# Kernel tuning notes

Measured on AMD Instinct MI355X. Metric: run time of the kernel, lower is better.

## Reference

```python
import jax, jax.numpy as jnp
import numpy as np

NUM_CLASSES = 1000  # label vocabulary size (matches fill_max for label)
B = 16384
D_IN = 1024   # image_embedding
D_OUT = 256   # projection_dim


def setup_inputs() -> dict:
    key = jax.random.key(0)
    k = jax.random.split(key, 6)
    x = jax.random.normal(k[0], (B, D_IN), dtype=jnp.float32)
    label = jax.random.randint(k[1], (B,), 0, NUM_CLASSES, dtype=jnp.int64)
    scale = 1.0 / np.sqrt(D_IN)
    W1_w = jax.random.normal(k[2], (D_OUT, D_IN), dtype=jnp.float32) * scale
    W1_b = jax.random.normal(k[3], (D_OUT,), dtype=jnp.float32) * scale
    W2_w = jax.random.normal(k[4], (D_OUT, D_IN), dtype=jnp.float32) * scale
    W2_b = jax.random.normal(k[5], (D_OUT,), dtype=jnp.float32) * scale
    return {"x": x, "label": label, "W1_w": W1_w, "W1_b": W1_b,
            "W2_w": W2_w, "W2_b": W2_b}


def reference(x, label, W1_w, W1_b, W2_w, W2_b):
    # Leave-one-group-out mean, vectorized via segment sums.
    # Original: for each i, mean of x[label != label_i] (detached); zeros if none.
    b = x.shape[0]
    xd = jax.lax.stop_gradient(x)  # .detach() in the torch code
    label_sum = jax.ops.segment_sum(xd, label, num_segments=NUM_CLASSES)          # [C, D_IN]
    label_cnt = jax.ops.segment_sum(jnp.ones((b,), dtype=x.dtype), label,
                                    num_segments=NUM_CLASSES)                     # [C]
    total_sum = xd.sum(axis=0)                                                    # [D_IN]
    other_sum = total_sum[None, :] - label_sum[label]                             # [B, D_IN]
    other_cnt = jnp.asarray(b, x.dtype) - label_cnt[label]                        # [B]
    calculate_mean = jnp.where(other_cnt[:, None] > 0,
                               other_sum / jnp.maximum(other_cnt, 1)[:, None],
                               jnp.zeros((), x.dtype))                            # [B, D_IN]
    # W1(x) + W2(calculate_mean)  (torch Linear: y = x @ W.T + b)
    return x @ W1_w.T + W1_b + calculate_mean @ W2_w.T + W2_b
```

## Files before the change

kernel.cpp:

```cpp
#include <hip/hip_runtime.h>

constexpr int B      = 16384;
constexpr int D_IN   = 1024;
constexpr int D_OUT  = 256;
constexpr int NCLS   = 1000;

constexpr size_t OFF_WB  = 0;
constexpr size_t OFF_V   = OFF_WB + (size_t)512 * D_IN * 2;
constexpr size_t OFF_U   = OFF_V  + (size_t)1024 * D_OUT * 4;
constexpr size_t OFF_CNT = OFF_U  + 4096;
constexpr size_t OFF_B12 = OFF_CNT + 4096;

typedef short bf16x8 __attribute__((ext_vector_type(8)));
typedef float f32x4  __attribute__((ext_vector_type(4)));

__device__ __forceinline__ unsigned short f2bf(float f) {
    unsigned int u = __float_as_uint(f);
    return (unsigned short)((u + 0x7FFFu + ((u >> 16) & 1u)) >> 16);
}

__device__ __forceinline__ void cvt8(const float4& a, const float4& b, unsigned short* dst) {
    union { unsigned short u[8]; bf16x8 v; } r;
    r.u[0] = f2bf(a.x); r.u[1] = f2bf(a.y); r.u[2] = f2bf(a.z); r.u[3] = f2bf(a.w);
    r.u[4] = f2bf(b.x); r.u[5] = f2bf(b.y); r.u[6] = f2bf(b.z); r.u[7] = f2bf(b.w);
    *(bf16x8*)dst = r.v;
}

__device__ __forceinline__ unsigned int cvtpk(float lo, float hi) {
    unsigned int r;
    asm volatile("v_cvt_pk_bf16_f32 %0, %1, %2" : "=v"(r) : "v"(lo), "v"(hi));
    return r;
}

__device__ __forceinline__ void async16(const void* g, void* l) {
    __builtin_amdgcn_global_load_lds(
        (const __attribute__((address_space(1))) void*)g,
        (__attribute__((address_space(3))) void*)l,
        16, 0, 0);
}

__device__ __forceinline__ bf16x8 packfrag(const float4& f0, const float4& f1) {
    union { unsigned int w[4]; bf16x8 v; } p;
    p.w[0] = cvtpk(f0.x, f0.y);
    p.w[1] = cvtpk(f0.z, f0.w);
    p.w[2] = cvtpk(f1.x, f1.y);
    p.w[3] = cvtpk(f1.z, f1.w);
    return p.v;
}

__global__ __launch_bounds__(256)
void prep_kernel(const float* __restrict__ W1, const float* __restrict__ W2,
                 const float* __restrict__ b1, const float* __restrict__ b2,
                 const int* __restrict__ label,
                 unsigned short* __restrict__ Wb,
                 float* __restrict__ V, float* __restrict__ U,
                 int* __restrict__ cnt, float* __restrict__ b12) {
    const int blk = blockIdx.x, tid = threadIdx.x;
    if (blk == 0) {
        __shared__ int h[1024];
#pragma unroll
        for (int q = 0; q < 4; ++q) h[q * 256 + tid] = 0;
        __syncthreads();
        for (int base = 0; base < 64; base += 16) {
            int lv[16];
#pragma unroll
            for (int u = 0; u < 16; ++u) lv[u] = label[(base + u) * 256 + tid];
#pragma unroll
            for (int u = 0; u < 16; ++u) atomicAdd(&h[lv[u]], 1);
        }
        __syncthreads();
#pragma unroll
        for (int q = 0; q < 4; ++q) cnt[q * 256 + tid] = h[q * 256 + tid];
        b12[tid] = b1[tid] + b2[tid];
    } else if (blk <= 128) {
        int lin = (blk - 1) * 256 + tid;
        int i = lin * 16;
        const float* src = (i < D_OUT * D_IN) ? (W1 + i) : (W2 + (i - D_OUT * D_IN));
        float4 a0 = *(const float4*)(src);
        float4 a1 = *(const float4*)(src + 4);
        float4 a2 = *(const float4*)(src + 8);
        float4 a3 = *(const float4*)(src + 12);
        cvt8(a0, a1, Wb + i);
        cvt8(a2, a3, Wb + i + 8);
    } else {
        int lb = blk - 129;
        int base = (lb * 256 + tid) * 16;
#pragma unroll
        for (int q = 0; q < 4; ++q)
            *(float4*)(V + base + q * 4) = float4{0.f, 0.f, 0.f, 0.f};
        if (lb == 0 && tid < 64)
            *(float4*)(U + tid * 4) = float4{0.f, 0.f, 0.f, 0.f};
    }
}


__global__ __launch_bounds__(256)
void gemm2_kernel(const float* __restrict__ x,
                  const unsigned short* __restrict__ Wb,
                  const int* __restrict__ label,
                  float* __restrict__ V, float* __restrict__ U) {
    __shared__ float Asf[64][64];
    __shared__ unsigned short Bs[64][64];

    const int tid  = threadIdx.x;
    const int bid  = blockIdx.x;
    const int xcd   = bid & 7;
    const int local = bid >> 3;
    const int bx = xcd * 32 + (local & 31);
    const int by = local >> 5;
    const int bm = bx * 64;
    const int bn = by * 64;

    const int wave = tid >> 6, lane = tid & 63;
    const int quad = lane >> 4, l16 = lane & 15;
    const int wm = (wave >> 1) * 32;
    const int wn = (wave & 1) * 32;
    const int sx = l16 & 7;

    const float* aps[4];
#pragma unroll
    for (int rr = 0; rr < 4; ++rr) {
        int dd = rr * 256 + tid;
        int r = dd >> 4, sl = dd & 15;
        int sc = sl ^ (r & 15);
        aps[rr] = x + (size_t)(bm + r) * D_IN + sc * 4;
    }
    const unsigned short* bps[2];
#pragma unroll
    for (int rr = 0; rr < 2; ++rr) {
        int dd = rr * 256 + tid;
        int r = dd >> 3, sl = dd & 7;
        int sc = sl ^ (r & 7);
        bps[rr] = Wb + (size_t)(256 + bn + r) * D_IN + sc * 8;
    }

    f32x4 acc[2][2] = {};

    for (int k0 = 0; k0 < D_IN; k0 += 64) {
        __syncthreads();
#pragma unroll
        for (int rr = 0; rr < 4; ++rr)
            async16(aps[rr] + k0, (char*)&Asf[0][0] + rr * 4096 + wave * 1024);
#pragma unroll
        for (int rr = 0; rr < 2; ++rr)
            async16(bps[rr] + k0, (char*)&Bs[0][0] + rr * 4096 + wave * 1024);
        __syncthreads();

#pragma unroll
        for (int ks = 0; ks < 2; ++ks) {
            const int s = ks * 4 + quad;
            bf16x8 af[2], bfr[2];
#pragma unroll
            for (int i = 0; i < 2; ++i) {
                const int row = wm + i * 16 + l16;
                float4 f0 = *(const float4*)&Asf[row][((2 * s) ^ l16) * 4];
                float4 f1 = *(const float4*)&Asf[row][((2 * s + 1) ^ l16) * 4];
                af[i] = packfrag(f0, f1);
            }
#pragma unroll
            for (int j = 0; j < 2; ++j)
                bfr[j] = *(const bf16x8*)&Bs[wn + j * 16 + l16][((s ^ sx) * 8)];
#pragma unroll
            for (int i = 0; i < 2; ++i)
#pragma unroll
                for (int j = 0; j < 2; ++j)
                    acc[i][j] = __builtin_amdgcn_mfma_f32_16x16x32_bf16(af[i], bfr[j], acc[i][j], 0, 0, 0);
        }
    }

    int lab[2][4];
#pragma unroll
    for (int i = 0; i < 2; ++i)
#pragma unroll
        for (int r = 0; r < 4; ++r)
            lab[i][r] = label[bm + wm + i * 16 + quad * 4 + r] * D_OUT;

#pragma unroll
    for (int j = 0; j < 2; ++j) {
        const int n = bn + wn + j * 16 + l16;
        float cs = 0.f;
#pragma unroll
        for (int i = 0; i < 2; ++i)
#pragma unroll
            for (int r = 0; r < 4; ++r) {
                float v = acc[i][j][r];
                cs += v;
                atomicAdd(&V[lab[i][r] + n], v);
            }
        cs += __shfl_xor(cs, 16);
        cs += __shfl_xor(cs, 32);
        if (quad == 0) atomicAdd(&U[n], cs);
    }
}

__global__ __launch_bounds__(256)
void gemm1_kernel(const float* __restrict__ x,
                  const unsigned short* __restrict__ Wb,
                  const int* __restrict__ label,
                  const float* __restrict__ V, const float* __restrict__ U,
                  const int* __restrict__ cnt, const float* __restrict__ b12,
                  float* __restrict__ out) {
    __shared__ float Asf[64][64];
    __shared__ unsigned short Bs[64][64];

    const int tid  = threadIdx.x;
    const int bid  = blockIdx.x;
    const int xcd   = bid & 7;
    const int local = bid >> 3;
    const int bx = xcd * 32 + (local & 31);
    const int by = local >> 5;
    const int bm = bx * 64;
    const int bn = by * 64;

    const int wave = tid >> 6, lane = tid & 63;
    const int quad = lane >> 4, l16 = lane & 15;
    const int wm = (wave >> 1) * 32;
    const int wn = (wave & 1) * 32;
    const int sx = l16 & 7;

    const float* aps[4];
#pragma unroll
    for (int rr = 0; rr < 4; ++rr) {
        int dd = rr * 256 + tid;
        int r = dd >> 4, sl = dd & 15;
        int sc = sl ^ (r & 15);
        aps[rr] = x + (size_t)(bm + r) * D_IN + sc * 4;
    }
    const unsigned short* bps[2];
#pragma unroll
    for (int rr = 0; rr < 2; ++rr) {
        int dd = rr * 256 + tid;
        int r = dd >> 3, sl = dd & 7;
        int sc = sl ^ (r & 7);
        bps[rr] = Wb + (size_t)(bn + r) * D_IN + sc * 8;
    }

    f32x4 acc[2][2] = {};

    for (int k0 = 0; k0 < D_IN; k0 += 64) {
        __syncthreads();
#pragma unroll
        for (int rr = 0; rr < 4; ++rr)
            async16(aps[rr] + k0, (char*)&Asf[0][0] + rr * 4096 + wave * 1024);
#pragma unroll
        for (int rr = 0; rr < 2; ++rr)
            async16(bps[rr] + k0, (char*)&Bs[0][0] + rr * 4096 + wave * 1024);
        __syncthreads();

#pragma unroll
        for (int ks = 0; ks < 2; ++ks) {
            const int s = ks * 4 + quad;
            bf16x8 af[2], bfr[2];
#pragma unroll
            for (int i = 0; i < 2; ++i) {
                const int row = wm + i * 16 + l16;
                float4 f0 = *(const float4*)&Asf[row][((2 * s) ^ l16) * 4];
                float4 f1 = *(const float4*)&Asf[row][((2 * s + 1) ^ l16) * 4];
                af[i] = packfrag(f0, f1);
            }
#pragma unroll
            for (int j = 0; j < 2; ++j)
                bfr[j] = *(const bf16x8*)&Bs[wn + j * 16 + l16][((s ^ sx) * 8)];
#pragma unroll
            for (int i = 0; i < 2; ++i)
#pragma unroll
                for (int j = 0; j < 2; ++j)
                    acc[i][j] = __builtin_amdgcn_mfma_f32_16x16x32_bf16(af[i], bfr[j], acc[i][j], 0, 0, 0);
        }
    }

    int lab[2][4];
    float inv[2][4];
#pragma unroll
    for (int i = 0; i < 2; ++i)
#pragma unroll
        for (int r = 0; r < 4; ++r) {
            const int m = bm + wm + i * 16 + quad * 4 + r;
            const int L = label[m];
            lab[i][r] = L * D_OUT;
            inv[i][r] = 1.0f / (float)(B - cnt[L]);
        }

#pragma unroll
    for (int j = 0; j < 2; ++j) {
        const int n = bn + wn + j * 16 + l16;
        const float un = U[n];
        const float bb = b12[n];
#pragma unroll
        for (int i = 0; i < 2; ++i)
#pragma unroll
            for (int r = 0; r < 4; ++r) {
                const int m = bm + wm + i * 16 + quad * 4 + r;
                out[(size_t)m * D_OUT + n] =
                    acc[i][j][r] + bb + (un - V[lab[i][r] + n]) * inv[i][r];
            }
    }
}

extern "C" void kernel_launch(void* const* d_in, const int* in_sizes, int n_in,
                              void* d_out, int out_size, void* d_ws, size_t ws_size,
                              hipStream_t stream) {
    const float* x    = (const float*)d_in[0];
    const int*   lab  = (const int*)d_in[1];
    const float* W1_w = (const float*)d_in[2];
    const float* W1_b = (const float*)d_in[3];
    const float* W2_w = (const float*)d_in[4];
    const float* W2_b = (const float*)d_in[5];
    float* out = (float*)d_out;

    char* ws = (char*)d_ws;
    unsigned short* Wb = (unsigned short*)(ws + OFF_WB);
    float* V   = (float*)(ws + OFF_V);
    float* U   = (float*)(ws + OFF_U);
    int*   cnt = (int*)(ws + OFF_CNT);
    float* b12 = (float*)(ws + OFF_B12);

    prep_kernel<<<193, 256, 0, stream>>>(W1_w, W2_w, W1_b, W2_b, lab, Wb, V, U, cnt, b12);
    gemm2_kernel<<<1024, 256, 0, stream>>>(x, Wb, lab, V, U);
    gemm1_kernel<<<1024, 256, 0, stream>>>(x, Wb, lab, V, U, cnt, b12, out);
}
```

Baseline: 164.8 us.

## Merge both GEMMs into one triple-buffered kernel with separate epilogue

The two GEMM kernels, which each read x from memory, become a single 2048-block GEMM over the concatenated 512-column weight. Blocks for the first half store raw x@W1 to a workspace buffer, and blocks for the second half do the segment atomics. The K loop now uses a 3-stage async-copy ring with explicit vmcnt waits and one barrier per step, so loads overlap with MFMA work. The block mapping groups the 8 column tiles of one row tile on the same XCD so x can be reused from L2. The cost is an extra 16 MB y1 write and read in a new elementwise epilogue kernel, plus triple-sized shared memory.

```diff
diff --git a/kernel.cpp b/kernel.cpp
--- a/kernel.cpp
+++ b/kernel.cpp
@@ -6,7 +6,8 @@
 constexpr int NCLS   = 1000;
 
 constexpr size_t OFF_WB  = 0;
-constexpr size_t OFF_V   = OFF_WB + (size_t)512 * D_IN * 2;
+constexpr size_t OFF_Y1  = OFF_WB + (size_t)512 * D_IN * 2;
+constexpr size_t OFF_V   = OFF_Y1 + (size_t)B * D_OUT * 4;
 constexpr size_t OFF_U   = OFF_V  + (size_t)1024 * D_OUT * 4;
 constexpr size_t OFF_CNT = OFF_U  + 4096;
 constexpr size_t OFF_B12 = OFF_CNT + 4096;
@@ -93,21 +94,21 @@
     }
 }
 
-
 __global__ __launch_bounds__(256)
-void gemm2_kernel(const float* __restrict__ x,
-                  const unsigned short* __restrict__ Wb,
-                  const int* __restrict__ label,
-                  float* __restrict__ V, float* __restrict__ U) {
-    __shared__ float Asf[64][64];
-    __shared__ unsigned short Bs[64][64];
+void gemm_kernel(const float* __restrict__ x,
+                 const unsigned short* __restrict__ Wb,
+                 const int* __restrict__ label,
+                 float* __restrict__ y1,
+                 float* __restrict__ V, float* __restrict__ U) {
+    __shared__ float Asf[3][64][64];
+    __shared__ unsigned short Bs[3][64][64];
 
     const int tid  = threadIdx.x;
     const int bid  = blockIdx.x;
     const int xcd   = bid & 7;
     const int local = bid >> 3;
-    const int bx = xcd * 32 + (local & 31);
-    const int by = local >> 5;
+    const int bx = xcd * 32 + (local >> 3);
+    const int by = local & 7;
     const int bm = bx * 64;
     const int bn = by * 64;
 
@@ -131,20 +132,32 @@
         int dd = rr * 256 + tid;
         int r = dd >> 3, sl = dd & 7;
         int sc = sl ^ (r & 7);
-        bps[rr] = Wb + (size_t)(256 + bn + r) * D_IN + sc * 8;
+        bps[rr] = Wb + (size_t)(bn + r) * D_IN + sc * 8;
     }
 
     f32x4 acc[2][2] = {};
 
-    for (int k0 = 0; k0 < D_IN; k0 += 64) {
-        __syncthreads();
+#pragma unroll
+    for (int t0 = 0; t0 < 2; ++t0) {
+        const int k0 = t0 * 64;
 #pragma unroll
         for (int rr = 0; rr < 4; ++rr)
-            async16(aps[rr] + k0, (char*)&Asf[0][0] + rr * 4096 + wave * 1024);
+            async16(aps[rr] + k0, (char*)&Asf[t0][0][0] + rr * 4096 + wave * 1024);
 #pragma unroll
         for (int rr = 0; rr < 2; ++rr)
-            async16(bps[rr] + k0, (char*)&Bs[0][0] + rr * 4096 + wave * 1024);
-        __syncthreads();
+            async16(bps[rr] + k0, (char*)&Bs[t0][0][0] + rr * 4096 + wave * 1024);
+    }
+
+#pragma unroll
+    for (int t = 0; t < 16; ++t) {
+        const int cur = t % 3;
+        if (t <= 14) {
+            asm volatile("s_waitcnt vmcnt(6)" ::: "memory");
+        } else {
+            asm volatile("s_waitcnt vmcnt(0)" ::: "memory");
+        }
+        __builtin_amdgcn_s_barrier();
+        __builtin_amdgcn_sched_barrier(0);
 
 #pragma unroll
         for (int ks = 0; ks < 2; ++ks) {
@@ -153,147 +166,98 @@
 #pragma unroll
             for (int i = 0; i < 2; ++i) {
                 const int row = wm + i * 16 + l16;
-                float4 f0 = *(const float4*)&Asf[row][((2 * s) ^ l16) * 4];
-                float4 f1 = *(const float4*)&Asf[row][((2 * s + 1) ^ l16) * 4];
+                float4 f0 = *(const float4*)&Asf[cur][row][((2 * s) ^ l16) * 4];
+                float4 f1 = *(const float4*)&Asf[cur][row][((2 * s + 1) ^ l16) * 4];
                 af[i] = packfrag(f0, f1);
             }
 #pragma unroll
             for (int j = 0; j < 2; ++j)
-                bfr[j] = *(const bf16x8*)&Bs[wn + j * 16 + l16][((s ^ sx) * 8)];
+                bfr[j] = *(const bf16x8*)&Bs[cur][wn + j * 16 + l16][((s ^ sx) * 8)];
 #pragma unroll
             for (int i = 0; i < 2; ++i)
 #pragma unroll
                 for (int j = 0; j < 2; ++j)
                     acc[i][j] = __builtin_amdgcn_mfma_f32_16x16x32_bf16(af[i], bfr[j], acc[i][j], 0, 0, 0);
         }
-    }
-
-    int lab[2][4];
-#pragma unroll
-    for (int i = 0; i < 2; ++i)
-#pragma unroll
-        for (int r = 0; r < 4; ++r)
-            lab[i][r] = label[bm + wm + i * 16 + quad * 4 + r] * D_OUT;
-
-#pragma unroll
-    for (int j = 0; j < 2; ++j) {
-        const int n = bn + wn + j * 16 + l16;
-        float cs = 0.f;
+
+        if (t <= 13) {
+            const int nb = (t + 2) % 3;
+            const int k2 = (t + 2) * 64;
+#pragma unroll
+            for (int rr = 0; rr < 4; ++rr)
+                async16(aps[rr] + k2, (char*)&Asf[nb][0][0] + rr * 4096 + wave * 1024);
+#pragma unroll
+            for (int rr = 0; rr < 2; ++rr)
+                async16(bps[rr] + k2, (char*)&Bs[nb][0][0] + rr * 4096 + wave * 1024);
+        }
+    }
+
+    if (by < 4) {
+#pragma unroll
+        for (int j = 0; j < 2; ++j) {
+            const int n = bn + wn + j * 16 + l16;
+#pragma unroll
+            for (int i = 0; i < 2; ++i)
+#pragma unroll
+                for (int r = 0; r < 4; ++r) {
+                    const int m = bm + wm + i * 16 + quad * 4 + r;
+                    y1[(size_t)m * D_OUT + n] = acc[i][j][r];
+                }
+        }
+    } else {
+        int lab[2][4];
 #pragma unroll
         for (int i = 0; i < 2; ++i)
 #pragma unroll
-            for (int r = 0; r < 4; ++r) {
-                float v = acc[i][j][r];
-                cs += v;
-                atomicAdd(&V[lab[i][r] + n], v);
-            }
-        cs += __shfl_xor(cs, 16);
-        cs += __shfl_xor(cs, 32);
-        if (quad == 0) atomicAdd(&U[n], cs);
+            for (int r = 0; r < 4; ++r)
+                lab[i][r] = label[bm + wm + i * 16 + quad * 4 + r] * D_OUT;
+
+        const int nb = bn - 256;
+#pragma unroll
+        for (int j = 0; j < 2; ++j) {
+            const int n = nb + wn + j * 16 + l16;
+            float cs = 0.f;
+#pragma unroll
+            for (int i = 0; i < 2; ++i)
+#pragma unroll
+                for (int r = 0; r < 4; ++r) {
+                    float v = acc[i][j][r];
+                    cs += v;
+                    atomicAdd(&V[lab[i][r] + n], v);
+                }
+            cs += __shfl_xor(cs, 16);
+            cs += __shfl_xor(cs, 32);
+            if (quad == 0) atomicAdd(&U[n], cs);
+        }
     }
 }
 
 __global__ __launch_bounds__(256)
-void gemm1_kernel(const float* __restrict__ x,
-                  const unsigned short* __restrict__ Wb,
-                  const int* __restrict__ label,
-                  const float* __restrict__ V, const float* __restrict__ U,
-                  const int* __restrict__ cnt, const float* __restrict__ b12,
-                  float* __restrict__ out) {
-    __shared__ float Asf[64][64];
-    __shared__ unsigned short Bs[64][64];
-
-    const int tid  = threadIdx.x;
-    const int bid  = blockIdx.x;
-    const int xcd   = bid & 7;
-    const int local = bid >> 3;
-    const int bx = xcd * 32 + (local & 31);
-    const int by = local >> 5;
-    const int bm = bx * 64;
-    const int bn = by * 64;
-
-    const int wave = tid >> 6, lane = tid & 63;
-    const int quad = lane >> 4, l16 = lane & 15;
-    const int wm = (wave >> 1) * 32;
-    const int wn = (wave & 1) * 32;
-    const int sx = l16 & 7;
-
-    const float* aps[4];
-#pragma unroll
-    for (int rr = 0; rr < 4; ++rr) {
-        int dd = rr * 256 + tid;
-        int r = dd >> 4, sl = dd & 15;
-        int sc = sl ^ (r & 15);
-        aps[rr] = x + (size_t)(bm + r) * D_IN + sc * 4;
-    }
-    const unsigned short* bps[2];
-#pragma unroll
-    for (int rr = 0; rr < 2; ++rr) {
-        int dd = rr * 256 + tid;
-        int r = dd >> 3, sl = dd & 7;
-        int sc = sl ^ (r & 7);
-        bps[rr] = Wb + (size_t)(bn + r) * D_IN + sc * 8;
-    }
-
-    f32x4 acc[2][2] = {};
-
-    for (int k0 = 0; k0 < D_IN; k0 += 64) {
-        __syncthreads();
-#pragma unroll
-        for (int rr = 0; rr < 4; ++rr)
-            async16(aps[rr] + k0, (char*)&Asf[0][0] + rr * 4096 + wave * 1024);
-#pragma unroll
-        for (int rr = 0; rr < 2; ++rr)
-            async16(bps[rr] + k0, (char*)&Bs[0][0] + rr * 4096 + wave * 1024);
-        __syncthreads();
-
-#pragma unroll
-        for (int ks = 0; ks < 2; ++ks) {
-            const int s = ks * 4 + quad;
-            bf16x8 af[2], bfr[2];
-#pragma unroll
-            for (int i = 0; i < 2; ++i) {
-                const int row = wm + i * 16 + l16;
-                float4 f0 = *(const float4*)&Asf[row][((2 * s) ^ l16) * 4];
-                float4 f1 = *(const float4*)&Asf[row][((2 * s + 1) ^ l16) * 4];
-                af[i] = packfrag(f0, f1);
-            }
-#pragma unroll
-            for (int j = 0; j < 2; ++j)
-                bfr[j] = *(const bf16x8*)&Bs[wn + j * 16 + l16][((s ^ sx) * 8)];
-#pragma unroll
-            for (int i = 0; i < 2; ++i)
-#pragma unroll
-                for (int j = 0; j < 2; ++j)
-                    acc[i][j] = __builtin_amdgcn_mfma_f32_16x16x32_bf16(af[i], bfr[j], acc[i][j], 0, 0, 0);
-        }
-    }
-
-    int lab[2][4];
-    float inv[2][4];
-#pragma unroll
-    for (int i = 0; i < 2; ++i)
-#pragma unroll
-        for (int r = 0; r < 4; ++r) {
-            const int m = bm + wm + i * 16 + quad * 4 + r;
-            const int L = label[m];
-            lab[i][r] = L * D_OUT;
-            inv[i][r] = 1.0f / (float)(B - cnt[L]);
-        }
-
-#pragma unroll
-    for (int j = 0; j < 2; ++j) {
-        const int n = bn + wn + j * 16 + l16;
-        const float un = U[n];
-        const float bb = b12[n];
-#pragma unroll
-        for (int i = 0; i < 2; ++i)
-#pragma unroll
-            for (int r = 0; r < 4; ++r) {
-                const int m = bm + wm + i * 16 + quad * 4 + r;
-                out[(size_t)m * D_OUT + n] =
-                    acc[i][j][r] + bb + (un - V[lab[i][r] + n]) * inv[i][r];
-            }
+void epi_kernel(const float* __restrict__ y1, const float* __restrict__ V,
+                const float* __restrict__ U, const float* __restrict__ b12,
+                const int* __restrict__ cnt, const int* __restrict__ label,
+                float* __restrict__ out) {
+    const int tid = threadIdx.x;
+    const int row = blockIdx.x * 64 + (tid >> 2);
+    const int lab = label[row];
+    const float inv = 1.0f / (float)(B - cnt[lab]);
+    const float* yp = y1 + (size_t)row * D_OUT;
+    const float* vp = V  + (size_t)lab * D_OUT;
+    float* op = out + (size_t)row * D_OUT;
+    const int c0 = (tid & 3) * 4;
+#pragma unroll
+    for (int it = 0; it < 16; ++it) {
+        const int c = c0 + it * 16;
+        float4 y = *(const float4*)(yp + c);
+        float4 v = *(const float4*)(vp + c);
+        float4 u = *(const float4*)(U + c);
+        float4 bb = *(const float4*)(b12 + c);
+        float4 o;
+        o.x = y.x + bb.x + (u.x - v.x) * inv;
+        o.y = y.y + bb.y + (u.y - v.y) * inv;
+        o.z = y.z + bb.z + (u.z - v.z) * inv;
+        o.w = y.w + bb.w + (u.w - v.w) * inv;
+        *(float4*)(op + c) = o;
     }
 }
 
@@ -310,12 +274,13 @@
 
     char* ws = (char*)d_ws;
     unsigned short* Wb = (unsigned short*)(ws + OFF_WB);
+    float* y1  = (float*)(ws + OFF_Y1);
     float* V   = (float*)(ws + OFF_V);
     float* U   = (float*)(ws + OFF_U);
     int*   cnt = (int*)(ws + OFF_CNT);
     float* b12 = (float*)(ws + OFF_B12);
 
     prep_kernel<<<193, 256, 0, stream>>>(W1_w, W2_w, W1_b, W2_b, lab, Wb, V, U, cnt, b12);
-    gemm2_kernel<<<1024, 256, 0, stream>>>(x, Wb, lab, V, U);
-    gemm1_kernel<<<1024, 256, 0, stream>>>(x, Wb, lab, V, U, cnt, b12, out);
-}
+    gemm_kernel<<<2048, 256, 0, stream>>>(x, Wb, lab, y1, V, U);
+    epi_kernel<<<B / 64, 256, 0, stream>>>(y1, V, U, b12, cnt, lab, out);
+}
```

Result: slower. 173.5 us (+5.3%).
